# Optimization experiments

Measured on AMD Instinct MI355X. Metric: run time of the kernel, lower is better.

The kernel has to match this reference:

```python
import jax, jax.numpy as jnp
import numpy as np

N = 50000
S = 4
HID = 64
E = 800000
IN_DIM = 2 + 8


def setup_inputs() -> dict:
    key = jax.random.key(0)
    ks = jax.random.split(key, 10)
    x = jax.random.normal(ks[0], (N, 3), dtype=jnp.float32)
    theta = jax.random.uniform(ks[1], (N,), dtype=jnp.float32) * np.pi
    H = jax.random.normal(ks[2], (N, S, 2), dtype=jnp.float32)
    edge_index = jax.random.randint(ks[3], (2, E), 0, N, dtype=jnp.int64)
    # MLP params (Linear stores weight as [out, in]; we use [in, out] layout here)
    def lin(k, fan_in, fan_out):
        bound = 1.0 / np.sqrt(fan_in)
        k1, k2 = jax.random.split(k)
        W = jax.random.uniform(k1, (fan_in, fan_out), minval=-bound, maxval=bound, dtype=jnp.float32)
        b = jax.random.uniform(k2, (fan_out,), minval=-bound, maxval=bound, dtype=jnp.float32)
        return W, b
    W1, b1 = lin(ks[4], IN_DIM, HID)
    W2, b2 = lin(ks[5], HID, HID)
    W3, b3 = lin(ks[6], HID, 2)
    return {"x": x, "theta": theta, "H": H, "edge_index": edge_index,
            "W1": W1, "b1": b1, "W2": W2, "b2": b2, "W3": W3, "b3": b3}


def reference(x, theta, H, edge_index, W1, b1, W2, b2, W3, b3):
    n_nodes = H.shape[0]
    i_idx = edge_index[0]
    j_idx = edge_index[1]

    dx = x[j_idx] - x[i_idx]                      # [E, 3]
    dz = dx[:, 2]
    r_3d = jnp.linalg.norm(dx, axis=-1)           # [E]
    r_xy = jnp.linalg.norm(dx[:, :2], axis=-1)    # [E]
    phi_ij = jnp.arctan2(dx[:, 1], dx[:, 0])
    theta_i = theta[i_idx]
    theta_j = theta[j_idx]
    delta_phi = phi_ij - theta_i
    delta_theta = theta_j - theta_i
    sin2dt = jnp.sin(2.0 * delta_theta)
    cos2dt = jnp.cos(2.0 * delta_theta)
    geom_feat = jnp.stack([
        r_3d, r_xy, dz,
        jnp.sin(delta_phi), jnp.cos(delta_phi),
        sin2dt, cos2dt,
        jnp.sign(dz) * sin2dt,
    ], axis=-1)                                    # [E, 8]

    # spin-2 rotation of H[j] into i's frame (angle = 2*(theta_j - theta_i))
    cos_a = cos2dt[:, None]                        # [E, 1]
    sin_a = sin2dt[:, None]
    H_j = H[j_idx]                                 # [E, S, 2]
    v_x, v_y = H_j[..., 0], H_j[..., 1]
    H_j_in_i = jnp.stack([cos_a * v_x - sin_a * v_y,
                          sin_a * v_x + cos_a * v_y], axis=-1)  # [E, S, 2]

    n_slots = H.shape[1]
    geom_expanded = jnp.broadcast_to(geom_feat[:, None, :], (geom_feat.shape[0], n_slots, 8))
    slot_input = jnp.concatenate([H_j_in_i, geom_expanded], axis=-1)  # [E, S, 10]

    h = jax.nn.silu(jnp.einsum('esd,dh->esh', slot_input, W1) + b1)
    h = jax.nn.silu(jnp.einsum('esh,hk->esk', h, W2) + b2)
    M = jnp.einsum('esk,ko->eso', h, W3) + b3       # [E, S, 2]

    H_new = jax.ops.segment_sum(M, i_idx, num_segments=n_nodes)  # [N, S, 2]
    return H_new
```

## Files before the change

kernel.cpp:

```cpp
#include <hip/hip_runtime.h>

#define EDGES 800000
#define GROUPS 10
#define EPB (GROUPS * 64)

typedef __attribute__((ext_vector_type(8))) short short8;
typedef __attribute__((ext_vector_type(4))) float f32x4;

__device__ __forceinline__ unsigned short f2bf(float f) {
    union { float f; unsigned u; } c; c.f = f;
    return (unsigned short)((c.u + 0x7FFFu + ((c.u >> 16) & 1u)) >> 16);
}

__device__ __forceinline__ unsigned pk2(float lo, float hi) {
    unsigned r;
    asm("v_cvt_pk_bf16_f32 %0, %1, %2" : "=v"(r) : "v"(lo), "v"(hi));
    return r;
}

__device__ __forceinline__ float silu_f(float t) {
    return t * __builtin_amdgcn_rcpf(1.0f + __expf(-t));
}

__device__ __forceinline__ float fast_atan2f(float y, float x) {
    float ax = __builtin_fabsf(x), ay = __builtin_fabsf(y);
    float mx = fmaxf(ax, ay), mn = fminf(ax, ay);
    float z  = mn * __builtin_amdgcn_rcpf(mx);
    float z2 = z * z;
    float p  = fmaf(z2, 0.0208351f, -0.0851330f);
    p = fmaf(z2, p, 0.1801410f);
    p = fmaf(z2, p, -0.3302995f);
    p = fmaf(z2, p, 0.9998660f);
    float t = z * p;
    t = (ay > ax)   ? 1.57079632679f - t : t;
    t = (x < 0.0f)  ? 3.14159265359f - t : t;
    t = (y < 0.0f)  ? -t : t;
    return (mx > 0.0f) ? t : 0.0f;
}

__global__ void detect_idx_kernel(const int* __restrict__ ei, int* __restrict__ flag) {
    int t = threadIdx.x;
    int v = 0;
    for (int k = t; k < 2048; k += 64) v |= ei[2 * k + 1];
    unsigned long long m = __ballot(v != 0);
    if (t == 0) flag[0] = (m != 0ull) ? 1 : 0;
}

__global__ __launch_bounds__(256, 2) void gnn_mfma_kernel(
    const float* __restrict__ x, const float* __restrict__ theta,
    const float* __restrict__ H, const int* __restrict__ ei,
    const float* __restrict__ W1, const float* __restrict__ b1,
    const float* __restrict__ W2, const float* __restrict__ b2,
    const float* __restrict__ W3, const float* __restrict__ b3,
    float* __restrict__ out, const int* __restrict__ flag)
{
    __shared__ unsigned short Xs[256 * 32];
    __shared__ int idxs[256];

    const int t    = threadIdx.x;
    const int lane = t & 63;
    const int wv   = t >> 6;
    const int g16  = lane >> 4;
    const int l15  = lane & 15;
    const bool idx32 = (flag[0] != 0);

    short8 w1f[4];
    #pragma unroll
    for (int nt = 0; nt < 4; ++nt) {
        short8 v;
        #pragma unroll
        for (int j = 0; j < 8; ++j) {
            int k = 8 * g16 + j;
            int h = nt * 16 + l15;
            float w = 0.0f;
            if (k < 10)       w = W1[k * 64 + h];
            else if (k == 10) w = b1[h];
            v[j] = (short)f2bf(w);
        }
        w1f[nt] = v;
    }
    short8 w2f[4][2];
    #pragma unroll
    for (int mt = 0; mt < 4; ++mt) {
        #pragma unroll
        for (int s = 0; s < 2; ++s) {
            short8 v;
            #pragma unroll
            for (int j = 0; j < 8; ++j) {
                int h1 = 16 * (2 * s + (j >> 2)) + 4 * g16 + (j & 3);
                int h2 = 16 * mt + l15;
                v[j] = (short)f2bf(W2[h1 * 64 + h2]);
            }
            w2f[mt][s] = v;
        }
    }
    short8 w3f[2];
    #pragma unroll
    for (int s = 0; s < 2; ++s) {
        short8 v;
        #pragma unroll
        for (int j = 0; j < 8; ++j) {
            int h2 = 16 * (2 * s + (j >> 2)) + 4 * g16 + (j & 3);
            float w = (l15 < 2) ? W3[h2 * 2 + l15] : 0.0f;
            v[j] = (short)f2bf(w);
        }
        w3f[s] = v;
    }
    f32x4 bias2[4];
    #pragma unroll
    for (int mt = 0; mt < 4; ++mt) {
        #pragma unroll
        for (int r = 0; r < 4; ++r)
            bias2[mt][r] = b2[16 * mt + 4 * g16 + r];
    }
    f32x4 c3i;
    #pragma unroll
    for (int r = 0; r < 4; ++r) {
        int o = 4 * g16 + r;
        c3i[r] = (o == 0) ? b3[0] : ((o == 1) ? b3[1] : 0.0f);
    }

    for (int grp = 0; grp < GROUPS; ++grp) {
        const int e0 = blockIdx.x * EPB + grp * 64;

        {
            int el = t >> 2, slot = t & 3;
            int e = e0 + el;
            int i, j;
            if (idx32) { i = ei[e];     j = ei[EDGES + e]; }
            else       { i = ei[2 * e]; j = ei[2 * EDGES + 2 * e]; }

            float dx0 = x[3 * j + 0] - x[3 * i + 0];
            float dx1 = x[3 * j + 1] - x[3 * i + 1];
            float dz  = x[3 * j + 2] - x[3 * i + 2];
            float rxy2 = dx0 * dx0 + dx1 * dx1;
            float r3d  = __builtin_amdgcn_sqrtf(rxy2 + dz * dz);
            float rxy  = __builtin_amdgcn_sqrtf(rxy2);
            float phi  = fast_atan2f(dx1, dx0);
            float ti = theta[i], tj = theta[j];
            float dphi = phi - ti;
            float sdp = __sinf(dphi), cdp = __cosf(dphi);
            float dt2 = 2.0f * (tj - ti);
            float s2 = __sinf(dt2), c2 = __cosf(dt2);
            float g7 = (dz > 0.0f) ? s2 : ((dz < 0.0f) ? -s2 : 0.0f);

            float2 hv = *(const float2*)&H[((long)j * 4 + slot) * 2];
            float in0 = c2 * hv.x - s2 * hv.y;
            float in1 = s2 * hv.x + c2 * hv.y;

            union { short8 s8; unsigned u[4]; } A, B;
            A.u[0] = pk2(in0, in1);
            A.u[1] = pk2(r3d, rxy);
            A.u[2] = pk2(dz, sdp);
            A.u[3] = pk2(cdp, s2);
            B.u[0] = pk2(c2, g7);
            B.u[1] = 0x00003F80u;
            B.u[2] = 0; B.u[3] = 0;
            short8 zz;
            #pragma unroll
            for (int q = 0; q < 8; ++q) zz[q] = 0;

            int row = t;
            unsigned short* bp = &Xs[row * 32];
            int sw = row & 3;
            *(short8*)(bp + ((0 ^ sw) << 3)) = A.s8;
            *(short8*)(bp + ((1 ^ sw) << 3)) = B.s8;
            *(short8*)(bp + ((2 ^ sw) << 3)) = zz;
            *(short8*)(bp + ((3 ^ sw) << 3)) = zz;
            idxs[row] = i * 8 + slot * 2;
        }
        __syncthreads();

        #pragma unroll
        for (int tt = 0; tt < 4; ++tt) {
            int row = wv * 64 + tt * 16 + l15;
            short8 xb = *(const short8*)(&Xs[row * 32] + ((g16 ^ (row & 3)) << 3));

            f32x4 z4 = {0.0f, 0.0f, 0.0f, 0.0f};
            f32x4 c1[4];
            #pragma unroll
            for (int nt = 0; nt < 4; ++nt)
                c1[nt] = __builtin_amdgcn_mfma_f32_16x16x32_bf16(w1f[nt], xb, z4, 0, 0, 0);

            short8 pb[2];
            #pragma unroll
            for (int s = 0; s < 2; ++s) {
                union { short8 s8; unsigned u[4]; } P;
                #pragma unroll
                for (int w = 0; w < 4; ++w) {
                    float lo = silu_f(c1[2 * s + (w >> 1)][(w & 1) * 2 + 0]);
                    float hi = silu_f(c1[2 * s + (w >> 1)][(w & 1) * 2 + 1]);
                    P.u[w] = pk2(lo, hi);
                }
                pb[s] = P.s8;
            }

            f32x4 c2a[4];
            #pragma unroll
            for (int mt = 0; mt < 4; ++mt) {
                f32x4 acc = __builtin_amdgcn_mfma_f32_16x16x32_bf16(w2f[mt][0], pb[0], bias2[mt], 0, 0, 0);
                acc       = __builtin_amdgcn_mfma_f32_16x16x32_bf16(w2f[mt][1], pb[1], acc,       0, 0, 0);
                c2a[mt] = acc;
            }

            short8 qb[2];
            #pragma unroll
            for (int s = 0; s < 2; ++s) {
                union { short8 s8; unsigned u[4]; } Q;
                #pragma unroll
                for (int w = 0; w < 4; ++w) {
                    float lo = silu_f(c2a[2 * s + (w >> 1)][(w & 1) * 2 + 0]);
                    float hi = silu_f(c2a[2 * s + (w >> 1)][(w & 1) * 2 + 1]);
                    Q.u[w] = pk2(lo, hi);
                }
                qb[s] = Q.s8;
            }

            f32x4 c3 = __builtin_amdgcn_mfma_f32_16x16x32_bf16(w3f[0], qb[0], c3i, 0, 0, 0);
            c3       = __builtin_amdgcn_mfma_f32_16x16x32_bf16(w3f[1], qb[1], c3,  0, 0, 0);

            if (g16 == 0) {
                int ob = idxs[row];
                atomicAdd(&out[ob + 0], c3[0]);
                atomicAdd(&out[ob + 1], c3[1]);
            }
        }
        __syncthreads();
    }
}

extern "C" void kernel_launch(void* const* d_in, const int* in_sizes, int n_in,
                              void* d_out, int out_size, void* d_ws, size_t ws_size,
                              hipStream_t stream) {
    const float* x     = (const float*)d_in[0];
    const float* theta = (const float*)d_in[1];
    const float* H     = (const float*)d_in[2];
    const int*   ei    = (const int*)d_in[3];
    const float* W1    = (const float*)d_in[4];
    const float* b1    = (const float*)d_in[5];
    const float* W2    = (const float*)d_in[6];
    const float* b2    = (const float*)d_in[7];
    const float* W3    = (const float*)d_in[8];
    const float* b3    = (const float*)d_in[9];
    float* out = (float*)d_out;

    hipMemsetAsync(d_out, 0, (size_t)out_size * sizeof(float), stream);

    int* flag = (int*)d_ws;
    detect_idx_kernel<<<1, 64, 0, stream>>>(ei, flag);

    gnn_mfma_kernel<<<EDGES / EPB, 256, 0, stream>>>(x, theta, H, ei,
                                                     W1, b1, W2, b2, W3, b3,
                                                     out, flag);
}
```

Baseline: 130.0 us.

## Double-buffer edge features in LDS and fold log2e into MLP weights

Splits the per-edge geometry and feature build into a helper and runs it for the next group while the MFMA MLP works on the current group. Ping-pong LDS buffers let the gather latency overlap with compute, and only one barrier is needed per group. The zero padding of the unused K columns is now written once up front instead of every iteration. It also pre-scales W1, b1 and b2 by log2(e) and W3 by ln(2), so SiLU can call exp2 directly without a multiply. The cost is twice the LDS footprint, more register pressure from the prefetch, and slightly different bf16 rounding of the scaled weights.

```diff
diff --git a/kernel.cpp b/kernel.cpp
--- a/kernel.cpp
+++ b/kernel.cpp
@@ -3,6 +3,9 @@
 #define EDGES 800000
 #define GROUPS 10
 #define EPB (GROUPS * 64)
+
+#define LOG2E 1.44269504089f
+#define LN2   0.69314718056f
 
 typedef __attribute__((ext_vector_type(8))) short short8;
 typedef __attribute__((ext_vector_type(4))) float f32x4;
@@ -18,8 +21,8 @@
     return r;
 }
 
-__device__ __forceinline__ float silu_f(float t) {
-    return t * __builtin_amdgcn_rcpf(1.0f + __expf(-t));
+__device__ __forceinline__ float silu_pre(float u) {
+    return u * __builtin_amdgcn_rcpf(1.0f + __builtin_amdgcn_exp2f(-u));
 }
 
 __device__ __forceinline__ float fast_atan2f(float y, float x) {
@@ -46,6 +49,51 @@
     if (t == 0) flag[0] = (m != 0ull) ? 1 : 0;
 }
 
+__device__ __forceinline__ void phase1_geom(
+    int e0, const float* __restrict__ x, const float* __restrict__ theta,
+    const float* __restrict__ H, const int* __restrict__ ei, bool idx32,
+    int t, unsigned short* __restrict__ XsBuf, int* __restrict__ idxBuf)
+{
+    int el = t >> 2, slot = t & 3;
+    int e = e0 + el;
+    int i, j;
+    if (idx32) { i = ei[e];     j = ei[EDGES + e]; }
+    else       { i = ei[2 * e]; j = ei[2 * EDGES + 2 * e]; }
+
+    float dx0 = x[3 * j + 0] - x[3 * i + 0];
+    float dx1 = x[3 * j + 1] - x[3 * i + 1];
+    float dz  = x[3 * j + 2] - x[3 * i + 2];
+    float rxy2 = dx0 * dx0 + dx1 * dx1;
+    float r3d  = __builtin_amdgcn_sqrtf(rxy2 + dz * dz);
+    float rxy  = __builtin_amdgcn_sqrtf(rxy2);
+    float phi  = fast_atan2f(dx1, dx0);
+    float ti = theta[i], tj = theta[j];
+    float dphi = phi - ti;
+    float sdp = __sinf(dphi), cdp = __cosf(dphi);
+    float dt2 = 2.0f * (tj - ti);
+    float s2 = __sinf(dt2), c2 = __cosf(dt2);
+    float g7 = (dz > 0.0f) ? s2 : ((dz < 0.0f) ? -s2 : 0.0f);
+
+    float2 hv = *(const float2*)&H[((long)j * 4 + slot) * 2];
+    float in0 = c2 * hv.x - s2 * hv.y;
+    float in1 = s2 * hv.x + c2 * hv.y;
+
+    union { short8 s8; unsigned u[4]; } A, B;
+    A.u[0] = pk2(in0, in1);
+    A.u[1] = pk2(r3d, rxy);
+    A.u[2] = pk2(dz, sdp);
+    A.u[3] = pk2(cdp, s2);
+    B.u[0] = pk2(c2, g7);
+    B.u[1] = 0x00003F80u;
+    B.u[2] = 0; B.u[3] = 0;
+
+    unsigned short* bp = XsBuf + t * 32;
+    int sw = t & 3;
+    *(short8*)(bp + ((0 ^ sw) << 3)) = A.s8;
+    *(short8*)(bp + ((1 ^ sw) << 3)) = B.s8;
+    idxBuf[t] = i * 8 + slot * 2;
+}
+
 __global__ __launch_bounds__(256, 2) void gnn_mfma_kernel(
     const float* __restrict__ x, const float* __restrict__ theta,
     const float* __restrict__ H, const int* __restrict__ ei,
@@ -54,8 +102,8 @@
     const float* __restrict__ W3, const float* __restrict__ b3,
     float* __restrict__ out, const int* __restrict__ flag)
 {
-    __shared__ unsigned short Xs[256 * 32];
-    __shared__ int idxs[256];
+    __shared__ unsigned short Xs[2][256 * 32];
+    __shared__ int idxs[2][256];
 
     const int t    = threadIdx.x;
     const int lane = t & 63;
@@ -64,6 +112,19 @@
     const int l15  = lane & 15;
     const bool idx32 = (flag[0] != 0);
 
+    {
+        short8 zz;
+        #pragma unroll
+        for (int q = 0; q < 8; ++q) zz[q] = 0;
+        #pragma unroll
+        for (int b = 0; b < 2; ++b) {
+            unsigned short* bp = &Xs[b][t * 32];
+            int sw = t & 3;
+            *(short8*)(bp + ((2 ^ sw) << 3)) = zz;
+            *(short8*)(bp + ((3 ^ sw) << 3)) = zz;
+        }
+    }
+
     short8 w1f[4];
     #pragma unroll
     for (int nt = 0; nt < 4; ++nt) {
@@ -73,8 +134,8 @@
             int k = 8 * g16 + j;
             int h = nt * 16 + l15;
             float w = 0.0f;
-            if (k < 10)       w = W1[k * 64 + h];
-            else if (k == 10) w = b1[h];
+            if (k < 10)       w = W1[k * 64 + h] * LOG2E;
+            else if (k == 10) w = b1[h] * LOG2E;
             v[j] = (short)f2bf(w);
         }
         w1f[nt] = v;
@@ -101,7 +162,7 @@
         #pragma unroll
         for (int j = 0; j < 8; ++j) {
             int h2 = 16 * (2 * s + (j >> 2)) + 4 * g16 + (j & 3);
-            float w = (l15 < 2) ? W3[h2 * 2 + l15] : 0.0f;
+            float w = (l15 < 2) ? W3[h2 * 2 + l15] * LN2 : 0.0f;
             v[j] = (short)f2bf(w);
         }
         w3f[s] = v;
@@ -111,7 +172,7 @@
     for (int mt = 0; mt < 4; ++mt) {
         #pragma unroll
         for (int r = 0; r < 4; ++r)
-            bias2[mt][r] = b2[16 * mt + 4 * g16 + r];
+            bias2[mt][r] = b2[16 * mt + 4 * g16 + r] * LOG2E;
     }
     f32x4 c3i;
     #pragma unroll
@@ -120,61 +181,23 @@
         c3i[r] = (o == 0) ? b3[0] : ((o == 1) ? b3[1] : 0.0f);
     }
 
+    phase1_geom(blockIdx.x * EPB, x, theta, H, ei, idx32, t, Xs[0], idxs[0]);
+    __syncthreads();
+
     for (int grp = 0; grp < GROUPS; ++grp) {
-        const int e0 = blockIdx.x * EPB + grp * 64;
-
-        {
-            int el = t >> 2, slot = t & 3;
-            int e = e0 + el;
-            int i, j;
-            if (idx32) { i = ei[e];     j = ei[EDGES + e]; }
-            else       { i = ei[2 * e]; j = ei[2 * EDGES + 2 * e]; }
-
-            float dx0 = x[3 * j + 0] - x[3 * i + 0];
-            float dx1 = x[3 * j + 1] - x[3 * i + 1];
-            float dz  = x[3 * j + 2] - x[3 * i + 2];
-            float rxy2 = dx0 * dx0 + dx1 * dx1;
-            float r3d  = __builtin_amdgcn_sqrtf(rxy2 + dz * dz);
-            float rxy  = __builtin_amdgcn_sqrtf(rxy2);
-            float phi  = fast_atan2f(dx1, dx0);
-            float ti = theta[i], tj = theta[j];
-            float dphi = phi - ti;
-            float sdp = __sinf(dphi), cdp = __cosf(dphi);
-            float dt2 = 2.0f * (tj - ti);
-            float s2 = __sinf(dt2), c2 = __cosf(dt2);
-            float g7 = (dz > 0.0f) ? s2 : ((dz < 0.0f) ? -s2 : 0.0f);
-
-            float2 hv = *(const float2*)&H[((long)j * 4 + slot) * 2];
-            float in0 = c2 * hv.x - s2 * hv.y;
-            float in1 = s2 * hv.x + c2 * hv.y;
-
-            union { short8 s8; unsigned u[4]; } A, B;
-            A.u[0] = pk2(in0, in1);
-            A.u[1] = pk2(r3d, rxy);
-            A.u[2] = pk2(dz, sdp);
-            A.u[3] = pk2(cdp, s2);
-            B.u[0] = pk2(c2, g7);
-            B.u[1] = 0x00003F80u;
-            B.u[2] = 0; B.u[3] = 0;
-            short8 zz;
-            #pragma unroll
-            for (int q = 0; q < 8; ++q) zz[q] = 0;
-
-            int row = t;
-            unsigned short* bp = &Xs[row * 32];
-            int sw = row & 3;
-            *(short8*)(bp + ((0 ^ sw) << 3)) = A.s8;
-            *(short8*)(bp + ((1 ^ sw) << 3)) = B.s8;
-            *(short8*)(bp + ((2 ^ sw) << 3)) = zz;
-            *(short8*)(bp + ((3 ^ sw) << 3)) = zz;
-            idxs[row] = i * 8 + slot * 2;
-        }
-        __syncthreads();
+        const int cur = grp & 1;
+
+        if (grp + 1 < GROUPS)
+            phase1_geom(blockIdx.x * EPB + (grp + 1) * 64, x, theta, H, ei,
+                        idx32, t, Xs[cur ^ 1], idxs[cur ^ 1]);
+
+        const unsigned short* Xc = Xs[cur];
+        const int* ic = idxs[cur];
 
         #pragma unroll
         for (int tt = 0; tt < 4; ++tt) {
             int row = wv * 64 + tt * 16 + l15;
-            short8 xb = *(const short8*)(&Xs[row * 32] + ((g16 ^ (row & 3)) << 3));
+            short8 xb = *(const short8*)(Xc + row * 32 + ((g16 ^ (row & 3)) << 3));
 
             f32x4 z4 = {0.0f, 0.0f, 0.0f, 0.0f};
             f32x4 c1[4];
@@ -188,8 +211,8 @@
                 union { short8 s8; unsigned u[4]; } P;
                 #pragma unroll
                 for (int w = 0; w < 4; ++w) {
-                    float lo = silu_f(c1[2 * s + (w >> 1)][(w & 1) * 2 + 0]);
-                    float hi = silu_f(c1[2 * s + (w >> 1)][(w & 1) * 2 + 1]);
+                    float lo = silu_pre(c1[2 * s + (w >> 1)][(w & 1) * 2 + 0]);
+                    float hi = silu_pre(c1[2 * s + (w >> 1)][(w & 1) * 2 + 1]);
                     P.u[w] = pk2(lo, hi);
                 }
                 pb[s] = P.s8;
@@ -209,8 +232,8 @@
                 union { short8 s8; unsigned u[4]; } Q;
                 #pragma unroll
                 for (int w = 0; w < 4; ++w) {
-                    float lo = silu_f(c2a[2 * s + (w >> 1)][(w & 1) * 2 + 0]);
-                    float hi = silu_f(c2a[2 * s + (w >> 1)][(w & 1) * 2 + 1]);
+                    float lo = silu_pre(c2a[2 * s + (w >> 1)][(w & 1) * 2 + 0]);
+                    float hi = silu_pre(c2a[2 * s + (w >> 1)][(w & 1) * 2 + 1]);
                     Q.u[w] = pk2(lo, hi);
                 }
                 qb[s] = Q.s8;
@@ -220,7 +243,7 @@
             c3       = __builtin_amdgcn_mfma_f32_16x16x32_bf16(w3f[1], qb[1], c3,  0, 0, 0);
 
             if (g16 == 0) {
-                int ob = idxs[row];
+                int ob = ic[row];
                 atomicAdd(&out[ob + 0], c3[0]);
                 atomicAdd(&out[ob + 1], c3[1]);
             }
```

After: 139.0 us. +6.9%, slower.
